# Performance work log

Hardware: AMD Instinct MI355X
Metric: run time of the kernel (lower is better)

The kernel has to match this reference:

```python
import jax, jax.numpy as jnp
import numpy as np
import math

D_MODEL = 1024
N_HEADS = 16
HEAD_DIM = D_MODEL // N_HEADS
FEAT = 16
WINDOW = 64
EPS_NORM = 1e-6
EPS_LIN = 1e-6
CHUNK = 128


def setup_inputs() -> dict:
    key = jax.random.key(0)
    ks = jax.random.split(key, 7)
    B, T = 2, 2048
    s = 0.02
    return {
        'x': jax.random.normal(ks[0], (B, T, D_MODEL), jnp.float32),
        'norm_w': jnp.ones((D_MODEL,), jnp.float32),
        'Wq': jax.random.normal(ks[1], (D_MODEL, D_MODEL), jnp.float32) * s,
        'Wk': jax.random.normal(ks[2], (D_MODEL, D_MODEL), jnp.float32) * s,
        'Wv': jax.random.normal(ks[3], (D_MODEL, D_MODEL), jnp.float32) * s,
        'Wqf': jax.random.normal(ks[4], (HEAD_DIM, FEAT), jnp.float32) * s,
        'Wkf': jax.random.normal(ks[5], (HEAD_DIM, FEAT), jnp.float32) * s,
        'Wout': jax.random.normal(ks[6], (2 * D_MODEL, D_MODEL), jnp.float32) * s,
    }


def rmsnorm(x, w):
    return x * jax.lax.rsqrt(jnp.mean(x * x, axis=-1, keepdims=True) + EPS_NORM) * w


def taylor_feature_map(x):
    # phi(x) = [1, x, x_i*x_j * (0.5 if i==j else 1/sqrt(2)) for i<=j]
    d = x.shape[-1]
    iu, ju = jnp.triu_indices(d)  # row-major (i, j>=i) matches torch loop order
    scale = jnp.where(iu == ju, 0.5, 1.0 / math.sqrt(2.0)).astype(x.dtype)
    quad = x[..., iu] * x[..., ju] * scale
    ones = jnp.ones(x.shape[:-1] + (1,), dtype=x.dtype)
    return jnp.concatenate([ones, x, quad], axis=-1)  # (..., 1+d+d(d+1)/2)


def linear_attention_causal(q_phi, k_phi, v):
    # Chunked-parallel causal linear attention: y_t = q_t @ KV_t / (q_t @ Ksum_t + eps)
    B, T, H, F = q_phi.shape
    D = v.shape[-1]
    Nc = T // CHUNK
    qc = q_phi.reshape(B, Nc, CHUNK, H, F).transpose(1, 0, 2, 3, 4)  # (Nc,B,C,H,F)
    kc = k_phi.reshape(B, Nc, CHUNK, H, F).transpose(1, 0, 2, 3, 4)
    vc = v.reshape(B, Nc, CHUNK, H, D).transpose(1, 0, 2, 3, 4)      # (Nc,B,C,H,D)
    causal = jnp.tril(jnp.ones((CHUNK, CHUNK), dtype=q_phi.dtype))   # include diagonal

    def step(carry, inp):
        kv, ksum = carry                      # (B,H,F,D), (B,H,F)
        qb, kb, vb = inp
        A = jnp.einsum('bchf,bshf->bhcs', qb, kb) * causal  # intra-chunk quadratic scores
        y = jnp.einsum('bhcs,bshd->bchd', A, vb) + jnp.einsum('bchf,bhfd->bchd', qb, kv)
        z = jnp.einsum('bhcs->bch', A) + jnp.einsum('bchf,bhf->bch', qb, ksum)
        kv = kv + jnp.einsum('bshf,bshd->bhfd', kb, vb)
        ksum = ksum + kb.sum(axis=1)
        return (kv, ksum), y / (z[..., None] + EPS_LIN)

    kv0 = jnp.zeros((B, H, F, D), dtype=q_phi.dtype)
    ks0 = jnp.zeros((B, H, F), dtype=q_phi.dtype)
    _, ys = jax.lax.scan(step, (kv0, ks0), (qc, kc, vc))
    return ys.transpose(1, 0, 2, 3, 4).reshape(B, T, H, D)


def sliding_window_attention(q, k, v):
    B, T, H, D = q.shape
    scale = 1.0 / math.sqrt(D)
    t = jnp.arange(T)
    allowed = (t[None, :] <= t[:, None]) & (t[None, :] >= t[:, None] - WINDOW)  # (T,T)
    scores = jnp.einsum('bqhd,bkhd->bhqk', q, k) * scale
    scores = jnp.where(allowed[None, None], scores, -jnp.inf)
    attn = jax.nn.softmax(scores, axis=-1)
    out = jnp.einsum('bhqk,bkhd->bqhd', attn, v)
    return out.reshape(B, T, H * D)


def reference(x, norm_w, Wq, Wk, Wv, Wqf, Wkf, Wout):
    B, T, _ = x.shape
    h = rmsnorm(x, norm_w)
    q = (h @ Wq).reshape(B, T, N_HEADS, HEAD_DIM)
    k = (h @ Wk).reshape(B, T, N_HEADS, HEAD_DIM)
    v = (h @ Wv).reshape(B, T, N_HEADS, HEAD_DIM)
    q_phi = taylor_feature_map(q @ Wqf)
    k_phi = taylor_feature_map(k @ Wkf)
    lin = linear_attention_causal(q_phi, k_phi, v).reshape(B, T, D_MODEL)
    win = sliding_window_attention(q, k, v)
    out = jnp.concatenate([lin, win], axis=-1) @ Wout
    return x + out
```

## Files before the change

### kernel.cpp

```cpp
#include <hip/hip_runtime.h>
#include <math.h>

#define BB 2
#define TT 2048
#define DM 1024
#define NH 16
#define HD 64
#define FEAT 16
#define WIN 64
#define RTOT (BB*TT)

typedef __bf16 bf16x8 __attribute__((ext_vector_type(8)));
typedef float  f32x4  __attribute__((ext_vector_type(4)));

__device__ __forceinline__ unsigned short f2bf(float f) {
    union { float f; unsigned u; } v; v.f = f;
    unsigned r = v.u + 0x7FFFu + ((v.u >> 16) & 1u);
    return (unsigned short)(r >> 16);
}
__device__ __forceinline__ float bf2f(unsigned short u) {
    union { unsigned u; float f; } v; v.u = ((unsigned)u) << 16; return v.f;
}

__device__ __forceinline__ void gl2lds16(const void* g, void* l) {
    __builtin_amdgcn_global_load_lds(
        (const __attribute__((address_space(1))) void*)g,
        (__attribute__((address_space(3))) void*)l, 16, 0, 0);
}

__global__ __launch_bounds__(256) void rmsnorm_kernel(const float* __restrict__ x,
                                                      const float* __restrict__ w,
                                                      unsigned short* __restrict__ h_bf) {
    int row = blockIdx.x;
    int tid = threadIdx.x;
    const float4* xr = (const float4*)(x + (size_t)row * DM);
    float4 xv = xr[tid];
    float ss = xv.x*xv.x + xv.y*xv.y + xv.z*xv.z + xv.w*xv.w;
    #pragma unroll
    for (int off = 32; off > 0; off >>= 1) ss += __shfl_down(ss, off, 64);
    __shared__ float red[4];
    if ((tid & 63) == 0) red[tid >> 6] = ss;
    __syncthreads();
    float tot = red[0] + red[1] + red[2] + red[3];
    float scale = rsqrtf(tot * (1.0f / DM) + 1e-6f);
    float4 wv = ((const float4*)w)[tid];
    ushort4 o;
    o.x = f2bf(xv.x * scale * wv.x);
    o.y = f2bf(xv.y * scale * wv.y);
    o.z = f2bf(xv.z * scale * wv.z);
    o.w = f2bf(xv.w * scale * wv.w);
    *(ushort4*)&h_bf[(size_t)row * DM + tid * 4] = o;
}

__global__ __launch_bounds__(256) void transpose_bf16_kernel(const float* __restrict__ W0,
                                                             const float* __restrict__ W1,
                                                             const float* __restrict__ W2,
                                                             const float* __restrict__ W3,
                                                             unsigned short* __restrict__ T0,
                                                             unsigned short* __restrict__ T1,
                                                             unsigned short* __restrict__ T2,
                                                             unsigned short* __restrict__ T3) {
    int z = blockIdx.z;
    int K = (z == 3) ? 2048 : 1024;
    const int N = 1024;
    if (blockIdx.y * 64 >= K) return;
    const float* W = (z == 0) ? W0 : (z == 1) ? W1 : (z == 2) ? W2 : W3;
    unsigned short* WT = (z == 0) ? T0 : (z == 1) ? T1 : (z == 2) ? T2 : T3;
    __shared__ float tile[64][65];
    int k0 = blockIdx.y * 64, n0 = blockIdx.x * 64;
    int t = threadIdx.x;
    int r = t >> 4, c4 = (t & 15) * 4;
    #pragma unroll
    for (int i = 0; i < 4; i++) {
        float4 vv = *(const float4*)&W[(size_t)(k0 + r + i*16) * N + n0 + c4];
        tile[r + i*16][c4 + 0] = vv.x;
        tile[r + i*16][c4 + 1] = vv.y;
        tile[r + i*16][c4 + 2] = vv.z;
        tile[r + i*16][c4 + 3] = vv.w;
    }
    __syncthreads();
    int rn = t >> 2, kq = (t & 3) * 16;
    unsigned short u[16];
    #pragma unroll
    for (int i = 0; i < 16; i++) u[i] = f2bf(tile[kq + i][rn]);
    size_t base = (size_t)(n0 + rn) * K + k0 + kq;
    *(uint4*)&WT[base]     = *(uint4*)&u[0];
    *(uint4*)&WT[base + 8] = *(uint4*)&u[8];
}

template<int LDA, int LDB>
__device__ __forceinline__ void gemm_core_db(const unsigned short* __restrict__ A,
                                             const unsigned short* __restrict__ BT,
                                             unsigned short* __restrict__ Cb,
                                             int k0g) {
    const int N = 1024;
    const int KITERS = 32;
    __shared__ __align__(16) unsigned short As[2 * 128 * 32];
    __shared__ __align__(16) unsigned short Bs[2 * 128 * 32];
    int tid = threadIdx.x;
    int lane = tid & 63;
    int w = tid >> 6;
    int wm = (w >> 1) * 64, wn = (w & 1) * 64;
    int m0 = blockIdx.y * 128, n0 = blockIdx.x * 128;
    int hi = lane >> 4;
    int l15 = lane & 15;

    int c0 = tid, c1 = tid + 256;
    int r0 = c0 >> 2, kh0 = ((c0 & 3) - (r0 >> 1)) & 3;
    int r1 = c1 >> 2, kh1 = ((c1 & 3) - (r1 >> 1)) & 3;
    const unsigned short* aP0 = A  + (size_t)(m0 + r0) * LDA + k0g + kh0 * 8;
    const unsigned short* aP1 = A  + (size_t)(m0 + r1) * LDA + k0g + kh1 * 8;
    const unsigned short* bP0 = BT + (size_t)(n0 + r0) * LDB + k0g + kh0 * 8;
    const unsigned short* bP1 = BT + (size_t)(n0 + r1) * LDB + k0g + kh1 * 8;
    unsigned short* asD0 = &As[c0 * 8];
    unsigned short* asD1 = &As[c1 * 8];
    unsigned short* bsD0 = &Bs[c0 * 8];
    unsigned short* bsD1 = &Bs[c1 * 8];

    int aOff[4], bOff[4];
    #pragma unroll
    for (int i = 0; i < 4; i++) {
        int m = wm + i * 16 + l15;
        aOff[i] = m * 32 + (((hi + (m >> 1)) & 3) * 8);
        int n = wn + i * 16 + l15;
        bOff[i] = n * 32 + (((hi + (n >> 1)) & 3) * 8);
    }

    f32x4 acc[4][4];
    #pragma unroll
    for (int i = 0; i < 4; i++)
        #pragma unroll
        for (int j = 0; j < 4; j++)
            acc[i][j] = (f32x4){0.f, 0.f, 0.f, 0.f};

    gl2lds16(aP0, asD0); gl2lds16(aP1, asD1);
    gl2lds16(bP0, bsD0); gl2lds16(bP1, bsD1);

    for (int it = 0; it < KITERS; it++) {
        int cur = (it & 1) * 4096;
        int nxt = 4096 - cur;
        __syncthreads();
        if (it + 1 < KITERS) {
            aP0 += 32; aP1 += 32; bP0 += 32; bP1 += 32;
            gl2lds16(aP0, asD0 + nxt); gl2lds16(aP1, asD1 + nxt);
            gl2lds16(bP0, bsD0 + nxt); gl2lds16(bP1, bsD1 + nxt);
        }
        bf16x8 af[4], bfr[4];
        #pragma unroll
        for (int i = 0; i < 4; i++) {
            af[i]  = *(const bf16x8*)&As[cur + aOff[i]];
            bfr[i] = *(const bf16x8*)&Bs[cur + bOff[i]];
        }
        #pragma unroll
        for (int i = 0; i < 4; i++)
            #pragma unroll
            for (int j = 0; j < 4; j++)
                acc[i][j] = __builtin_amdgcn_mfma_f32_16x16x32_bf16(af[i], bfr[j], acc[i][j], 0, 0, 0);
    }
    #pragma unroll
    for (int i = 0; i < 4; i++) {
        #pragma unroll
        for (int j = 0; j < 4; j++) {
            int col = n0 + wn + j * 16 + l15;
            #pragma unroll
            for (int r = 0; r < 4; r++) {
                int row = m0 + wm + i * 16 + hi * 4 + r;
                Cb[(size_t)row * N + col] = f2bf(acc[i][j][r]);
            }
        }
    }
}

__global__ __launch_bounds__(256) void gemm_qkv_mfma(const unsigned short* __restrict__ A,
                                                     const unsigned short* __restrict__ BT0,
                                                     const unsigned short* __restrict__ BT1,
                                                     const unsigned short* __restrict__ BT2,
                                                     unsigned short* __restrict__ C0,
                                                     unsigned short* __restrict__ C1,
                                                     unsigned short* __restrict__ C2) {
    const unsigned short* BT = (blockIdx.z == 0) ? BT0 : (blockIdx.z == 1) ? BT1 : BT2;
    unsigned short* C = (blockIdx.z == 0) ? C0 : (blockIdx.z == 1) ? C1 : C2;
    gemm_core_db<1024, 1024>(A, BT, C, 0);
}

__global__ __launch_bounds__(256) void gemm_out_mfma(const unsigned short* __restrict__ A,
                                                     const unsigned short* __restrict__ BT,
                                                     unsigned short* __restrict__ P0,
                                                     unsigned short* __restrict__ P1) {
    unsigned short* P = (blockIdx.z == 0) ? P0 : P1;
    gemm_core_db<2048, 2048>(A, BT, P, blockIdx.z * 1024);
}

__global__ __launch_bounds__(256) void out_reduce_kernel(const float* __restrict__ x,
                                                         const unsigned short* __restrict__ P0,
                                                         const unsigned short* __restrict__ P1,
                                                         float* __restrict__ out) {
    int g = blockIdx.x * 256 + threadIdx.x;
    size_t e = (size_t)g * 4;
    float4 xv = *(const float4*)&x[e];
    ushort4 a = *(const ushort4*)&P0[e];
    ushort4 b = *(const ushort4*)&P1[e];
    float4 o;
    o.x = xv.x + bf2f(a.x) + bf2f(b.x);
    o.y = xv.y + bf2f(a.y) + bf2f(b.y);
    o.z = xv.z + bf2f(a.z) + bf2f(b.z);
    o.w = xv.w + bf2f(a.w) + bf2f(b.w);
    *(float4*)&out[e] = o;
}

__global__ __launch_bounds__(256) void feat_kernel(const unsigned short* __restrict__ qb,
                                                   const unsigned short* __restrict__ kb,
                                                   const float* __restrict__ Wqf,
                                                   const float* __restrict__ Wkf,
                                                   unsigned short* __restrict__ qf,
                                                   unsigned short* __restrict__ kf) {
    __shared__ float Wl[HD * FEAT];
    const unsigned short* src = blockIdx.z ? kb : qb;
    const float* Wm = blockIdx.z ? Wkf : Wqf;
    unsigned short* dst = blockIdx.z ? kf : qf;
    int tid = threadIdx.x;
    ((float4*)Wl)[tid] = ((const float4*)Wm)[tid];
    __syncthreads();
    int gid = blockIdx.x * 256 + tid;
    int f = gid & 15;
    int rowh = gid >> 4;
    const unsigned short* s = src + (size_t)rowh * HD;
    float acc = 0.f;
    #pragma unroll
    for (int d = 0; d < HD; d++) acc += bf2f(s[d]) * Wl[d * FEAT + f];
    dst[gid] = f2bf(acc);
}

__global__ __launch_bounds__(256) void win_mfma_kernel(const unsigned short* __restrict__ q_bf,
                                                       const unsigned short* __restrict__ k_bf,
                                                       const unsigned short* __restrict__ v_bf,
                                                       unsigned short* __restrict__ cat_bf) {
    int qtile = blockIdx.x;
    int bh = blockIdx.y;
    int h = bh & 15;
    int b = bh >> 4;
    int tid = threadIdx.x;
    int lane = tid & 63;
    int wv = tid >> 6;
    int qr0 = wv * 16;
    int t0 = qtile * 64;
    int k0 = t0 - 64;

    __shared__ __align__(16) unsigned short Qs[64 * 64];
    __shared__ __align__(16) unsigned short Ks[128 * 64];
    __shared__ __align__(16) unsigned short Vt[64 * 128];
    __shared__ __align__(16) unsigned short Pl[64 * 128];

    #pragma unroll
    for (int half = 0; half < 2; half++) {
        int slot = tid + half * 256;
        int row = slot >> 3, pos = slot & 7;
        int o = (pos - row) & 7;
        gl2lds16(q_bf + (size_t)(b * TT + t0 + row) * (NH * HD) + h * HD + o * 8,
                 &Qs[slot * 8]);
    }
    #pragma unroll
    for (int qd = 0; qd < 4; qd++) {
        int slot = tid + qd * 256;
        int row = slot >> 3, pos = slot & 7;
        int o = (pos - row) & 7;
        int kg = k0 + row;
        if (kg >= 0) {
            gl2lds16(k_bf + (size_t)(b * TT + kg) * (NH * HD) + h * HD + o * 8,
                     &Ks[slot * 8]);
        } else {
            uint4 z = {0, 0, 0, 0};
            *(uint4*)&Ks[slot * 8] = z;
        }
    }
    {
        int kk = tid & 127;
        int dh = tid >> 7;
        int kg = k0 + kk;
        unsigned short tmp[32];
        if (kg >= 0) {
            size_t base = (size_t)(b * TT + kg) * (NH * HD) + h * HD + dh * 32;
            *(uint4*)&tmp[0]  = *(const uint4*)&v_bf[base];
            *(uint4*)&tmp[8]  = *(const uint4*)&v_bf[base + 8];
            *(uint4*)&tmp[16] = *(const uint4*)&v_bf[base + 16];
            *(uint4*)&tmp[24] = *(const uint4*)&v_bf[base + 24];
        } else {
            #pragma unroll
            for (int d = 0; d < 32; d++) tmp[d] = 0;
        }
        int o = kk >> 3, klow = kk & 7;
        #pragma unroll
        for (int d = 0; d < 32; d++) {
            int dim = dh * 32 + d;
            Vt[dim * 128 + ((o + dim) & 15) * 8 + klow] = tmp[d];
        }
    }
    __syncthreads();

    int hi = lane >> 4;
    int lan15 = lane & 15;
    f32x4 sc[8];
    #pragma unroll
    for (int nt = 0; nt < 8; nt++) sc[nt] = (f32x4){0.f, 0.f, 0.f, 0.f};
    #pragma unroll
    for (int ks = 0; ks < 2; ks++) {
        int m = qr0 + lan15;
        int oA = ks * 4 + hi;
        bf16x8 a = *(const bf16x8*)&Qs[m * 64 + ((oA + m) & 7) * 8];
        #pragma unroll
        for (int nt = 0; nt < 8; nt++) {
            int n = nt * 16 + lan15;
            bf16x8 bb = *(const bf16x8*)&Ks[n * 64 + ((oA + n) & 7) * 8];
            sc[nt] = __builtin_amdgcn_mfma_f32_16x16x32_bf16(a, bb, sc[nt], 0, 0, 0);
        }
    }

    float lrow[4];
    #pragma unroll
    for (int r = 0; r < 4; r++) {
        int tq = t0 + qr0 + hi * 4 + r;
        float mx = -1e30f;
        #pragma unroll
        for (int nt = 0; nt < 8; nt++) {
            int s = k0 + nt * 16 + lan15;
            bool ok = (s >= 0) && (s <= tq) && (s >= tq - WIN);
            float vv = ok ? sc[nt][r] * 0.125f : -1e30f;
            sc[nt][r] = vv;
            mx = fmaxf(mx, vv);
        }
        #pragma unroll
        for (int off = 1; off < 16; off <<= 1) mx = fmaxf(mx, __shfl_xor(mx, off, 64));
        float ls = 0.f;
        #pragma unroll
        for (int nt = 0; nt < 8; nt++) {
            float e = __expf(sc[nt][r] - mx);
            sc[nt][r] = e;
            ls += e;
        }
        #pragma unroll
        for (int off = 1; off < 16; off <<= 1) ls += __shfl_xor(ls, off, 64);
        lrow[r] = ls;
    }

    #pragma unroll
    for (int nt = 0; nt < 8; nt++) {
        #pragma unroll
        for (int r = 0; r < 4; r++) {
            int row = qr0 + hi * 4 + r;
            int col = nt * 16 + lan15;
            Pl[row * 128 + (((col >> 3) + row) & 15) * 8 + (col & 7)] = f2bf(sc[nt][r]);
        }
    }
    __syncthreads();

    f32x4 y[4];
    #pragma unroll
    for (int nt = 0; nt < 4; nt++) y[nt] = (f32x4){0.f, 0.f, 0.f, 0.f};
    #pragma unroll
    for (int ks = 0; ks < 4; ks++) {
        int m = qr0 + lan15;
        int oA = ks * 4 + hi;
        bf16x8 a = *(const bf16x8*)&Pl[m * 128 + ((oA + m) & 15) * 8];
        #pragma unroll
        for (int nt = 0; nt < 4; nt++) {
            int n = nt * 16 + lan15;
            bf16x8 bb = *(const bf16x8*)&Vt[n * 128 + ((oA + n) & 15) * 8];
            y[nt] = __builtin_amdgcn_mfma_f32_16x16x32_bf16(a, bb, y[nt], 0, 0, 0);
        }
    }

    #pragma unroll
    for (int nt = 0; nt < 4; nt++) {
        #pragma unroll
        for (int r = 0; r < 4; r++) {
            int row = qr0 + hi * 4 + r;
            int dim = nt * 16 + lan15;
            cat_bf[(size_t)(b * TT + t0 + row) * (2 * DM) + DM + h * HD + dim] =
                f2bf(y[nt][r] / lrow[r]);
        }
    }
}

#define PHI 160
#define NCH 32
#define KVROWS 65
#define CH_STRIDE ((size_t)32 * KVROWS * PHI)

__global__ __launch_bounds__(256) void lin_kv_kernel(const unsigned short* __restrict__ kf,
                                                     const unsigned short* __restrict__ v_bf,
                                                     unsigned short* __restrict__ kvbuf) {
    int c = blockIdx.x, bh = blockIdx.y;
    int h = bh & 15, b = bh >> 4;
    int tid = threadIdx.x, lane = tid & 63, w = tid >> 6;
    int hi = lane >> 4, l15 = lane & 15;

    __shared__ unsigned short kf_l[64 * 16];
    __shared__ __align__(16) unsigned short PhiT[192 * 76];
    __shared__ __align__(16) unsigned short Vt[80 * 64];
    __shared__ unsigned short iu[136], ju[136];
    __shared__ float sclut[136];

    if (tid < 136) {
        int qq = tid, i = 0;
        while (qq >= 16 - i) { qq -= 16 - i; i++; }
        iu[tid] = (unsigned short)i; ju[tid] = (unsigned short)(i + qq);
        sclut[tid] = (qq == 0) ? 0.5f : 0.70710678118654752f;
    }
    {
        int r = tid >> 2, f4 = (tid & 3) * 4;
        *(ushort4*)&kf_l[r * 16 + f4] =
            *(const ushort4*)&kf[((size_t)((b * TT + c * 64 + r) * NH + h)) * FEAT + f4];
    }
    {
        int p = tid & 31, dq = (tid >> 5) * 8;
        size_t base0 = ((size_t)(b * TT + c * 64 + 2 * p)) * DM + h * HD + dq;
        unsigned short a[8], bq[8];
        *(uint4*)a  = *(const uint4*)&v_bf[base0];
        *(uint4*)bq = *(const uint4*)&v_bf[base0 + DM];
        int colo = p >> 2, coll = (2 * p) & 7;
        #pragma unroll
        for (int d = 0; d < 8; d++) {
            int row = dq + d;
            ushort2 u; u.x = a[d]; u.y = bq[d];
            *(ushort2*)&Vt[row * 64 + ((colo + row) & 7) * 8 + coll] = u;
        }
        #pragma unroll
        for (int i = 0; i < 4; i++) {
            int e = tid + i * 256;
            Vt[(64 + (e >> 6)) * 64 + (e & 63)] = 0x3F80;
        }
    }
    __syncthreads();
    {
        int s = tid & 63, fb = tid >> 6;
        const unsigned short* krow = &kf_l[s * 16];
        for (int it = 0; it < 40; it++) {
            int f = fb * 40 + it;
            float val;
            if (f == 0) val = 1.f;
            else if (f < 17) val = bf2f(krow[f - 1]);
            else if (f < 153) { int qq = f - 17; val = bf2f(krow[iu[qq]]) * bf2f(krow[ju[qq]]) * sclut[qq]; }
            else val = 0.f;
            PhiT[f * 76 + s] = f2bf(val);
        }
    }
    __syncthreads();
    f32x4 acc[5][3];
    #pragma unroll
    for (int m = 0; m < 5; m++)
        #pragma unroll
        for (int j = 0; j < 3; j++) acc[m][j] = (f32x4){0.f, 0.f, 0.f, 0.f};
    #pragma unroll
    for (int ks = 0; ks < 2; ks++) {
        bf16x8 bfrag[3];
        #pragma unroll
        for (int j = 0; j < 3; j++)
            bfrag[j] = *(const bf16x8*)&PhiT[((3 * w + j) * 16 + l15) * 76 + ks * 32 + hi * 8];
        #pragma unroll
        for (int m = 0; m < 5; m++) {
            int mrow = m * 16 + l15;
            bf16x8 afrag = *(const bf16x8*)&Vt[mrow * 64 + (((ks * 4 + hi) + mrow) & 7) * 8];
            #pragma unroll
            for (int j = 0; j < 3; j++)
                acc[m][j] = __builtin_amdgcn_mfma_f32_16x16x32_bf16(afrag, bfrag[j], acc[m][j], 0, 0, 0);
        }
    }
    size_t obase = ((size_t)c * 32 + bh) * (KVROWS * PHI);
    #pragma unroll
    for (int m = 0; m < 5; m++) {
        #pragma unroll
        for (int j = 0; j < 3; j++) {
            int f = (3 * w + j) * 16 + l15;
            if (f >= PHI) continue;
            #pragma unroll
            for (int r = 0; r < 4; r++) {
                int row = m * 16 + hi * 4 + r;
                if (row >= KVROWS) continue;
                kvbuf[obase + row * PHI + f] = f2bf(acc[m][j][r]);
            }
        }
    }
}

__global__ __launch_bounds__(256) void lin_scan_kernel(unsigned short* __restrict__ kvbuf) {
    int e = blockIdx.x * 256 + threadIdx.x;
    int bh = blockIdx.y;
    if (e >= KVROWS * PHI) return;
    float acc = 0.f;
    size_t off = (size_t)bh * (KVROWS * PHI) + e;
    for (int c = 0; c < NCH; c++) {
        float vv = bf2f(kvbuf[off]);
        kvbuf[off] = f2bf(acc);
        acc += vv;
        off += CH_STRIDE;
    }
}

__global__ __launch_bounds__(256) void lin_out_kernel(const unsigned short* __restrict__ qf,
                                                      const unsigned short* __restrict__ kf,
                                                      const unsigned short* __restrict__ v_bf,
                                                      const unsigned short* __restrict__ kvbuf,
                                                      unsigned short* __restrict__ cat_bf) {
    int c = blockIdx.x, bh = blockIdx.y;
    int h = bh & 15, b = bh >> 4;
    int tid = threadIdx.x, lane = tid & 63, w = tid >> 6;
    int hi = lane >> 4, l15 = lane & 15;

    __shared__ unsigned short qf_l[64 * 16];
    __shared__ __align__(16) unsigned short kf_lb[64 * 34];
    __shared__ __align__(16) unsigned short KVS_l[80 * 164];
    __shared__ __align__(16) unsigned short Vt[80 * 64];
    __shared__ __align__(16) unsigned short Phi_l[64 * 164];
    __shared__ __align__(16) unsigned short P_l[64 * 64];
    __shared__ unsigned short iu[136], ju[136];
    __shared__ float sclut[136];

    if (tid < 136) {
        int qq = tid, i = 0;
        while (qq >= 16 - i) { qq -= 16 - i; i++; }
        iu[tid] = (unsigned short)i; ju[tid] = (unsigned short)(i + qq);
        sclut[tid] = (qq == 0) ? 0.5f : 0.70710678118654752f;
    }
    {
        int r = tid >> 2, f4 = (tid & 3) * 4;
        *(ushort4*)&qf_l[r * 16 + f4] =
            *(const ushort4*)&qf[((size_t)((b * TT + c * 64 + r) * NH + h)) * FEAT + f4];
    }
    {
        int r = tid >> 2, f4 = (tid & 3) * 4;
        *(ushort4*)&kf_lb[r * 34 + f4] =
            *(const ushort4*)&kf[((size_t)((b * TT + c * 64 + r) * NH + h)) * FEAT + f4];
        ushort4 z4 = {0, 0, 0, 0};
        *(ushort4*)&kf_lb[r * 34 + 16 + f4] = z4;
    }
    {
        int p = tid & 31, dq = (tid >> 5) * 8;
        size_t base0 = ((size_t)(b * TT + c * 64 + 2 * p)) * DM + h * HD + dq;
        unsigned short a[8], bq[8];
        *(uint4*)a  = *(const uint4*)&v_bf[base0];
        *(uint4*)bq = *(const uint4*)&v_bf[base0 + DM];
        int colo = p >> 2, coll = (2 * p) & 7;
        #pragma unroll
        for (int d = 0; d < 8; d++) {
            int row = dq + d;
            ushort2 u; u.x = a[d]; u.y = bq[d];
            *(ushort2*)&Vt[row * 64 + ((colo + row) & 7) * 8 + coll] = u;
        }
        #pragma unroll
        for (int i = 0; i < 4; i++) {
            int e = tid + i * 256;
            Vt[(64 + (e >> 6)) * 64 + (e & 63)] = 0x3F80;
        }
    }
    {
        size_t gbase = ((size_t)c * 32 + bh) * (KVROWS * PHI);
        #pragma unroll
        for (int i = 0; i < 11; i++) {
            int e4 = tid + i * 256;
            if (e4 < KVROWS * 40) {
                int r = e4 / 40, q4 = (e4 % 40) * 4;
                *(ushort4*)&KVS_l[r * 164 + q4] =
                    *(const ushort4*)&kvbuf[gbase + r * PHI + q4];
            }
        }
        #pragma unroll
        for (int i = 0; i < 3; i++) {
            int e4 = tid + i * 256;
            if (e4 < 15 * 40) {
                int r = 65 + e4 / 40, q4 = (e4 % 40) * 4;
                ushort4 z4 = {0, 0, 0, 0};
                *(ushort4*)&KVS_l[r * 164 + q4] = z4;
            }
        }
    }
    __syncthreads();

    {
        int s = tid & 63, fb = tid >> 6;
        const unsigned short* qrow = &qf_l[s * 16];
        for (int it = 0; it < 40; it++) {
            int f = fb * 40 + it;
            float val;
            if (f == 0) val = 1.f;
            else if (f < 17) val = bf2f(qrow[f - 1]);
            else if (f < 153) { int qq = f - 17; val = bf2f(qrow[iu[qq]]) * bf2f(qrow[ju[qq]]) * sclut[qq]; }
            else val = 0.f;
            Phi_l[s * 164 + f] = f2bf(val);
        }
    }
    __syncthreads();

    f32x4 acc[5];
    #pragma unroll
    for (int n = 0; n < 5; n++) acc[n] = (f32x4){0.f, 0.f, 0.f, 0.f};

    int t_m = w * 16 + l15;

    #pragma unroll
    for (int ks = 0; ks < 5; ks++) {
        bf16x8 af = *(const bf16x8*)&Phi_l[t_m * 164 + ks * 32 + hi * 8];
        #pragma unroll
        for (int n = 0; n < 5; n++) {
            bf16x8 bb = *(const bf16x8*)&KVS_l[(n * 16 + l15) * 164 + ks * 32 + hi * 8];
            acc[n] = __builtin_amdgcn_mfma_f32_16x16x32_bf16(af, bb, acc[n], 0, 0, 0);
        }
    }

    {
        union { unsigned short u[8]; bf16x8 v; } aq;
        #pragma unroll
        for (int j = 0; j < 8; j++) {
            int f = hi * 8 + j;
            aq.u[j] = (f < 16) ? qf_l[t_m * 16 + f] : (unsigned short)0;
        }
        #pragma unroll
        for (int n = 0; n < 4; n++) {
            bf16x8 bk = *(const bf16x8*)&kf_lb[(n * 16 + l15) * 34 + hi * 8];
            f32x4 zv = {0.f, 0.f, 0.f, 0.f};
            f32x4 sc = __builtin_amdgcn_mfma_f32_16x16x32_bf16(aq.v, bk, zv, 0, 0, 0);
            int sl = n * 16 + l15;
            #pragma unroll
            for (int r = 0; r < 4; r++) {
                int rl = w * 16 + hi * 4 + r;
                float sv = 1.f + 0.5f * sc[r];
                sv = sv * sv;
                if (sl > rl) sv = 0.f;
                P_l[rl * 64 + (((sl >> 3) + rl) & 7) * 8 + (sl & 7)] = f2bf(sv);
            }
        }
    }
    __syncthreads();

    #pragma unroll
    for (int ks = 0; ks < 2; ks++) {
        int oA = ks * 4 + hi;
        bf16x8 a = *(const bf16x8*)&P_l[t_m * 64 + ((oA + t_m) & 7) * 8];
        #pragma unroll
        for (int n = 0; n < 5; n++) {
            int nrow = n * 16 + l15;
            bf16x8 bb = *(const bf16x8*)&Vt[nrow * 64 + ((oA + nrow) & 7) * 8];
            acc[n] = __builtin_amdgcn_mfma_f32_16x16x32_bf16(a, bb, acc[n], 0, 0, 0);
        }
    }

    #pragma unroll
    for (int r = 0; r < 4; r++) {
        float zz = __shfl(acc[4][r], (lane & 48), 64);
        int token = c * 64 + w * 16 + hi * 4 + r;
        #pragma unroll
        for (int n = 0; n < 4; n++) {
            int d = n * 16 + l15;
            cat_bf[((size_t)(b * TT + token)) * (2 * DM) + h * HD + d] =
                f2bf(acc[n][r] / (zz + 1e-6f));
        }
    }
}

extern "C" void kernel_launch(void* const* d_in, const int* in_sizes, int n_in,
                              void* d_out, int out_size, void* d_ws, size_t ws_size,
                              hipStream_t stream) {
    const float* x      = (const float*)d_in[0];
    const float* norm_w = (const float*)d_in[1];
    const float* Wq     = (const float*)d_in[2];
    const float* Wk     = (const float*)d_in[3];
    const float* Wv     = (const float*)d_in[4];
    const float* Wqf    = (const float*)d_in[5];
    const float* Wkf    = (const float*)d_in[6];
    const float* Wout   = (const float*)d_in[7];
    float* out = (float*)d_out;

    char* p = (char*)d_ws;
    unsigned short* h_bf = (unsigned short*)p; p += (size_t)RTOT * DM * 2;
    unsigned short* WqT  = (unsigned short*)p; p += (size_t)DM * DM * 2;
    unsigned short* WkT  = (unsigned short*)p; p += (size_t)DM * DM * 2;
    unsigned short* WvT  = (unsigned short*)p; p += (size_t)DM * DM * 2;
    unsigned short* WoT  = (unsigned short*)p; p += (size_t)DM * 2 * DM * 2;
    unsigned short* q_bf = (unsigned short*)p; p += (size_t)RTOT * DM * 2;
    unsigned short* k_bf = (unsigned short*)p; p += (size_t)RTOT * DM * 2;
    unsigned short* v_bf = (unsigned short*)p; p += (size_t)RTOT * DM * 2;
    unsigned short* qf_bf = (unsigned short*)p; p += (size_t)RTOT * NH * FEAT * 2;
    unsigned short* kf_bf = (unsigned short*)p; p += (size_t)RTOT * NH * FEAT * 2;
    unsigned short* cat_bf = (unsigned short*)p; p += (size_t)RTOT * 2 * DM * 2;
    unsigned short* kvbuf  = (unsigned short*)p; p += (size_t)NCH * 32 * KVROWS * PHI * 2;
    unsigned short* P0 = (unsigned short*)p; p += (size_t)RTOT * DM * 2;
    unsigned short* P1 = (unsigned short*)p; p += (size_t)RTOT * DM * 2;

    rmsnorm_kernel<<<RTOT, 256, 0, stream>>>(x, norm_w, h_bf);
    transpose_bf16_kernel<<<dim3(16, 32, 4), 256, 0, stream>>>(Wq, Wk, Wv, Wout, WqT, WkT, WvT, WoT);
    gemm_qkv_mfma<<<dim3(8, 32, 3), 256, 0, stream>>>(h_bf, WqT, WkT, WvT, q_bf, k_bf, v_bf);
    feat_kernel<<<dim3((RTOT * NH * FEAT) / 256, 1, 2), 256, 0, stream>>>(q_bf, k_bf, Wqf, Wkf, qf_bf, kf_bf);
    win_mfma_kernel<<<dim3(TT / 64, BB * NH), 256, 0, stream>>>(q_bf, k_bf, v_bf, cat_bf);
    lin_kv_kernel<<<dim3(NCH, BB * NH), 256, 0, stream>>>(kf_bf, v_bf, kvbuf);
    lin_scan_kernel<<<dim3((KVROWS * PHI + 255) / 256, BB * NH), 256, 0, stream>>>(kvbuf);
    lin_out_kernel<<<dim3(NCH, BB * NH), 256, 0, stream>>>(qf_bf, kf_bf, v_bf, kvbuf, cat_bf);
    gemm_out_mfma<<<dim3(8, 32, 2), 256, 0, stream>>>(cat_bf, WoT, P0, P1);
    out_reduce_kernel<<<RTOT * DM / 1024, 256, 0, stream>>>(x, P0, P1, out);
}
```

Baseline: 268.1 us.

## Use 256x256 GEMM tiles with triple-buffered LDS and 4-way split-K output

```diff
diff --git a/kernel.cpp b/kernel.cpp
--- a/kernel.cpp
+++ b/kernel.cpp
@@ -88,77 +88,94 @@
     *(uint4*)&WT[base + 8] = *(uint4*)&u[8];
 }
 
-template<int LDA, int LDB>
-__device__ __forceinline__ void gemm_core_db(const unsigned short* __restrict__ A,
+template<int LD, int KITERS>
+__device__ __forceinline__ void gemm256_core(const unsigned short* __restrict__ A,
                                              const unsigned short* __restrict__ BT,
                                              unsigned short* __restrict__ Cb,
                                              int k0g) {
     const int N = 1024;
-    const int KITERS = 32;
-    __shared__ __align__(16) unsigned short As[2 * 128 * 32];
-    __shared__ __align__(16) unsigned short Bs[2 * 128 * 32];
+    __shared__ __align__(16) unsigned short As[3 * 256 * 32];
+    __shared__ __align__(16) unsigned short Bs[3 * 256 * 32];
     int tid = threadIdx.x;
     int lane = tid & 63;
     int w = tid >> 6;
-    int wm = (w >> 1) * 64, wn = (w & 1) * 64;
-    int m0 = blockIdx.y * 128, n0 = blockIdx.x * 128;
+    int wm = (w >> 2) * 128, wn = (w & 3) * 64;
+    int m0 = blockIdx.y * 256, n0 = blockIdx.x * 256;
     int hi = lane >> 4;
     int l15 = lane & 15;
 
-    int c0 = tid, c1 = tid + 256;
+    int c0 = tid, c1 = tid + 512;
     int r0 = c0 >> 2, kh0 = ((c0 & 3) - (r0 >> 1)) & 3;
     int r1 = c1 >> 2, kh1 = ((c1 & 3) - (r1 >> 1)) & 3;
-    const unsigned short* aP0 = A  + (size_t)(m0 + r0) * LDA + k0g + kh0 * 8;
-    const unsigned short* aP1 = A  + (size_t)(m0 + r1) * LDA + k0g + kh1 * 8;
-    const unsigned short* bP0 = BT + (size_t)(n0 + r0) * LDB + k0g + kh0 * 8;
-    const unsigned short* bP1 = BT + (size_t)(n0 + r1) * LDB + k0g + kh1 * 8;
+    const unsigned short* aP0 = A  + (size_t)(m0 + r0) * LD + k0g + kh0 * 8;
+    const unsigned short* aP1 = A  + (size_t)(m0 + r1) * LD + k0g + kh1 * 8;
+    const unsigned short* bP0 = BT + (size_t)(n0 + r0) * LD + k0g + kh0 * 8;
+    const unsigned short* bP1 = BT + (size_t)(n0 + r1) * LD + k0g + kh1 * 8;
     unsigned short* asD0 = &As[c0 * 8];
     unsigned short* asD1 = &As[c1 * 8];
     unsigned short* bsD0 = &Bs[c0 * 8];
     unsigned short* bsD1 = &Bs[c1 * 8];
 
-    int aOff[4], bOff[4];
-    #pragma unroll
-    for (int i = 0; i < 4; i++) {
+    int aOff[8], bOff[4];
+    #pragma unroll
+    for (int i = 0; i < 8; i++) {
         int m = wm + i * 16 + l15;
         aOff[i] = m * 32 + (((hi + (m >> 1)) & 3) * 8);
-        int n = wn + i * 16 + l15;
-        bOff[i] = n * 32 + (((hi + (n >> 1)) & 3) * 8);
-    }
-
-    f32x4 acc[4][4];
-    #pragma unroll
-    for (int i = 0; i < 4; i++)
+    }
+    #pragma unroll
+    for (int j = 0; j < 4; j++) {
+        int n = wn + j * 16 + l15;
+        bOff[j] = n * 32 + (((hi + (n >> 1)) & 3) * 8);
+    }
+
+    f32x4 acc[8][4];
+    #pragma unroll
+    for (int i = 0; i < 8; i++)
         #pragma unroll
         for (int j = 0; j < 4; j++)
             acc[i][j] = (f32x4){0.f, 0.f, 0.f, 0.f};
 
-    gl2lds16(aP0, asD0); gl2lds16(aP1, asD1);
-    gl2lds16(bP0, bsD0); gl2lds16(bP1, bsD1);
-
-    for (int it = 0; it < KITERS; it++) {
-        int cur = (it & 1) * 4096;
-        int nxt = 4096 - cur;
-        __syncthreads();
-        if (it + 1 < KITERS) {
-            aP0 += 32; aP1 += 32; bP0 += 32; bP1 += 32;
-            gl2lds16(aP0, asD0 + nxt); gl2lds16(aP1, asD1 + nxt);
-            gl2lds16(bP0, bsD0 + nxt); gl2lds16(bP1, bsD1 + nxt);
-        }
-        bf16x8 af[4], bfr[4];
-        #pragma unroll
-        for (int i = 0; i < 4; i++) {
-            af[i]  = *(const bf16x8*)&As[cur + aOff[i]];
-            bfr[i] = *(const bf16x8*)&Bs[cur + bOff[i]];
-        }
-        #pragma unroll
-        for (int i = 0; i < 4; i++)
+#define STAGE256(ts, bf) do {                                   \
+        int _o = (ts) * 32;                                     \
+        int _b = (bf) * 8192;                                   \
+        gl2lds16(aP0 + _o, asD0 + _b);                          \
+        gl2lds16(aP1 + _o, asD1 + _b);                          \
+        gl2lds16(bP0 + _o, bsD0 + _b);                          \
+        gl2lds16(bP1 + _o, bsD1 + _b);                          \
+    } while (0)
+
+    STAGE256(0, 0);
+    STAGE256(1, 1);
+
+    for (int t = 0; t < KITERS; t++) {
+        int rd = t % 3;
+        if (t + 1 < KITERS) {
+            asm volatile("s_waitcnt vmcnt(4)" ::: "memory");
+        } else {
+            asm volatile("s_waitcnt vmcnt(0)" ::: "memory");
+        }
+        __builtin_amdgcn_s_barrier();
+        asm volatile("" ::: "memory");
+        if (t + 2 < KITERS) STAGE256(t + 2, (t + 2) % 3);
+        const unsigned short* Ab = &As[rd * 8192];
+        const unsigned short* Bb = &Bs[rd * 8192];
+        bf16x8 af[8], bfr[4];
+        #pragma unroll
+        for (int i = 0; i < 8; i++) af[i] = *(const bf16x8*)&Ab[aOff[i]];
+        #pragma unroll
+        for (int j = 0; j < 4; j++) bfr[j] = *(const bf16x8*)&Bb[bOff[j]];
+        __builtin_amdgcn_s_setprio(1);
+        #pragma unroll
+        for (int i = 0; i < 8; i++)
             #pragma unroll
             for (int j = 0; j < 4; j++)
                 acc[i][j] = __builtin_amdgcn_mfma_f32_16x16x32_bf16(af[i], bfr[j], acc[i][j], 0, 0, 0);
-    }
-    #pragma unroll
-    for (int i = 0; i < 4; i++) {
+        __builtin_amdgcn_s_setprio(0);
+    }
+#undef STAGE256
+
+    #pragma unroll
+    for (int i = 0; i < 8; i++) {
         #pragma unroll
         for (int j = 0; j < 4; j++) {
             int col = n0 + wn + j * 16 + l15;
@@ -171,40 +188,47 @@
     }
 }
 
-__global__ __launch_bounds__(256) void gemm_qkv_mfma(const unsigned short* __restrict__ A,
-                                                     const unsigned short* __restrict__ BT0,
-                                                     const unsigned short* __restrict__ BT1,
-                                                     const unsigned short* __restrict__ BT2,
-                                                     unsigned short* __restrict__ C0,
-                                                     unsigned short* __restrict__ C1,
-                                                     unsigned short* __restrict__ C2) {
+__global__ __launch_bounds__(512, 2) void gemm_qkv_mfma(const unsigned short* __restrict__ A,
+                                                        const unsigned short* __restrict__ BT0,
+                                                        const unsigned short* __restrict__ BT1,
+                                                        const unsigned short* __restrict__ BT2,
+                                                        unsigned short* __restrict__ C0,
+                                                        unsigned short* __restrict__ C1,
+                                                        unsigned short* __restrict__ C2) {
     const unsigned short* BT = (blockIdx.z == 0) ? BT0 : (blockIdx.z == 1) ? BT1 : BT2;
     unsigned short* C = (blockIdx.z == 0) ? C0 : (blockIdx.z == 1) ? C1 : C2;
-    gemm_core_db<1024, 1024>(A, BT, C, 0);
-}
-
-__global__ __launch_bounds__(256) void gemm_out_mfma(const unsigned short* __restrict__ A,
-                                                     const unsigned short* __restrict__ BT,
-                                                     unsigned short* __restrict__ P0,
-                                                     unsigned short* __restrict__ P1) {
-    unsigned short* P = (blockIdx.z == 0) ? P0 : P1;
-    gemm_core_db<2048, 2048>(A, BT, P, blockIdx.z * 1024);
+    gemm256_core<1024, 32>(A, BT, C, 0);
+}
+
+__global__ __launch_bounds__(512, 2) void gemm_out_mfma(const unsigned short* __restrict__ A,
+                                                        const unsigned short* __restrict__ BT,
+                                                        unsigned short* __restrict__ P0,
+                                                        unsigned short* __restrict__ P1,
+                                                        unsigned short* __restrict__ P2,
+                                                        unsigned short* __restrict__ P3) {
+    unsigned short* P = (blockIdx.z == 0) ? P0 : (blockIdx.z == 1) ? P1
+                      : (blockIdx.z == 2) ? P2 : P3;
+    gemm256_core<2048, 16>(A, BT, P, blockIdx.z * 512);
 }
 
 __global__ __launch_bounds__(256) void out_reduce_kernel(const float* __restrict__ x,
                                                          const unsigned short* __restrict__ P0,
                                                          const unsigned short* __restrict__ P1,
+                                                         const unsigned short* __restrict__ P2,
+                                                         const unsigned short* __restrict__ P3,
                                                          float* __restrict__ out) {
     int g = blockIdx.x * 256 + threadIdx.x;
     size_t e = (size_t)g * 4;
     float4 xv = *(const float4*)&x[e];
     ushort4 a = *(const ushort4*)&P0[e];
     ushort4 b = *(const ushort4*)&P1[e];
+    ushort4 c = *(const ushort4*)&P2[e];
+    ushort4 d = *(const ushort4*)&P3[e];
     float4 o;
-    o.x = xv.x + bf2f(a.x) + bf2f(b.x);
-    o.y = xv.y + bf2f(a.y) + bf2f(b.y);
-    o.z = xv.z + bf2f(a.z) + bf2f(b.z);
-    o.w = xv.w + bf2f(a.w) + bf2f(b.w);
+    o.x = xv.x + bf2f(a.x) + bf2f(b.x) + bf2f(c.x) + bf2f(d.x);
+    o.y = xv.y + bf2f(a.y) + bf2f(b.y) + bf2f(c.y) + bf2f(d.y);
+    o.z = xv.z + bf2f(a.z) + bf2f(b.z) + bf2f(c.z) + bf2f(d.z);
+    o.w = xv.w + bf2f(a.w) + bf2f(b.w) + bf2f(c.w) + bf2f(d.w);
     *(float4*)&out[e] = o;
 }
 
@@ -684,15 +708,17 @@
     unsigned short* kvbuf  = (unsigned short*)p; p += (size_t)NCH * 32 * KVROWS * PHI * 2;
     unsigned short* P0 = (unsigned short*)p; p += (size_t)RTOT * DM * 2;
     unsigned short* P1 = (unsigned short*)p; p += (size_t)RTOT * DM * 2;
+    unsigned short* P2 = h_bf;
+    unsigned short* P3 = q_bf;
 
     rmsnorm_kernel<<<RTOT, 256, 0, stream>>>(x, norm_w, h_bf);
     transpose_bf16_kernel<<<dim3(16, 32, 4), 256, 0, stream>>>(Wq, Wk, Wv, Wout, WqT, WkT, WvT, WoT);
-    gemm_qkv_mfma<<<dim3(8, 32, 3), 256, 0, stream>>>(h_bf, WqT, WkT, WvT, q_bf, k_bf, v_bf);
+    gemm_qkv_mfma<<<dim3(4, 16, 3), 512, 0, stream>>>(h_bf, WqT, WkT, WvT, q_bf, k_bf, v_bf);
     feat_kernel<<<dim3((RTOT * NH * FEAT) / 256, 1, 2), 256, 0, stream>>>(q_bf, k_bf, Wqf, Wkf, qf_bf, kf_bf);
     win_mfma_kernel<<<dim3(TT / 64, BB * NH), 256, 0, stream>>>(q_bf, k_bf, v_bf, cat_bf);
     lin_kv_kernel<<<dim3(NCH, BB * NH), 256, 0, stream>>>(kf_bf, v_bf, kvbuf);
     lin_scan_kernel<<<dim3((KVROWS * PHI + 255) / 256, BB * NH), 256, 0, stream>>>(kvbuf);
     lin_out_kernel<<<dim3(NCH, BB * NH), 256, 0, stream>>>(qf_bf, kf_bf, v_bf, kvbuf, cat_bf);
-    gemm_out_mfma<<<dim3(8, 32, 2), 256, 0, stream>>>(cat_bf, WoT, P0, P1);
-    out_reduce_kernel<<<RTOT * DM / 1024, 256, 0, stream>>>(x, P0, P1, out);
-}
+    gemm_out_mfma<<<dim3(4, 16, 4), 512, 0, stream>>>(cat_bf, WoT, P0, P1, P2, P3);
+    out_reduce_kernel<<<RTOT * DM / 1024, 256, 0, stream>>>(x, P0, P1, P2, P3, out);
+}
```

After: 268.4 us. No clear change (+0.1%).
